# Kernel tuning notes

Hardware: AMD Instinct MI355X
Metric: run time of the kernel (lower is better)

The kernel has to match this reference:

```python
import jax, jax.numpy as jnp
import numpy as np
from jax import lax

SPARSE_TH = 0.01
STRIDE = (1, 1)


def setup_inputs() -> dict:
    key = jax.random.key(0)
    k1, k2, k3 = jax.random.split(key, 3)
    x = jax.random.normal(k1, (32, 56, 56, 256), dtype=jnp.float32)  # NHWC
    # weight: (out_channels, in_channels, kh, kw); scale so a fraction falls below sparse_th
    weight = jax.random.normal(k2, (256, 256, 3, 3), dtype=jnp.float32) * 0.05
    bias = jax.random.normal(k3, (256,), dtype=jnp.float32)
    return {"x": x, "weight": weight, "bias": bias}


def reference(x, weight, bias):
    # Threshold weights: |w| < sparse_th -> 0 (the sparse kernel computes the
    # identical math as a dense valid conv with the masked weight)
    w = jnp.where(jnp.abs(weight) < SPARSE_TH, jnp.zeros_like(weight), weight)
    # OIHW -> HWIO for NHWC conv
    w_hwio = jnp.transpose(w, (2, 3, 1, 0))
    out = lax.conv_general_dilated(
        x, w_hwio,
        window_strides=STRIDE,
        padding="VALID",
        dimension_numbers=("NHWC", "HWIO", "NHWC"),
    )
    return out + bias.reshape(1, 1, 1, -1)
```

## Files before the change

### kernel.cpp

```cpp
#include <hip/hip_runtime.h>
#include <hip/hip_bf16.h>


typedef __bf16 bf16x8 __attribute__((ext_vector_type(8)));
typedef float f32x4 __attribute__((ext_vector_type(4)));

#define GLOBAL_AS __attribute__((address_space(1)))
#define LDS_AS __attribute__((address_space(3)))

static __device__ __forceinline__ void glds16(const void* g, void* l) {
    __builtin_amdgcn_global_load_lds((const GLOBAL_AS unsigned int*)g,
                                     (LDS_AS unsigned int*)l, 16, 0, 0);
}

static __device__ __forceinline__ unsigned short f2bf(float f) {
    unsigned int u = __float_as_uint(f);
    unsigned int r = u + 0x7FFFu + ((u >> 16) & 1u);
    return (unsigned short)(r >> 16);
}

__global__ void cvt_xw(const float* __restrict__ x, unsigned short* __restrict__ xb,
                       const float* __restrict__ w, unsigned short* __restrict__ wt) {
    const int NXB = 32 * 56 * 56 * 256 / (256 * 8);
    if (blockIdx.x < NXB) {
        int i = (blockIdx.x * 256 + threadIdx.x) * 8;
        const float4* p = (const float4*)(x + i);
        float4 a = p[0], b = p[1];
        uint4 v;
        v.x = (unsigned)f2bf(a.x) | ((unsigned)f2bf(a.y) << 16);
        v.y = (unsigned)f2bf(a.z) | ((unsigned)f2bf(a.w) << 16);
        v.z = (unsigned)f2bf(b.x) | ((unsigned)f2bf(b.y) << 16);
        v.w = (unsigned)f2bf(b.z) | ((unsigned)f2bf(b.w) << 16);
        *(uint4*)(xb + i) = v;
    } else {
        int co = blockIdx.x - NXB;
        int ci = threadIdx.x;
        const float* src = w + co * 2304 + ci * 9;
        unsigned short* dst = wt + co * 2304 + ci;
#pragma unroll
        for (int khw = 0; khw < 9; ++khw) {
            float v = src[khw];
            v = (fabsf(v) < 0.01f) ? 0.0f : v;
            dst[khw * 256] = f2bf(v);
        }
    }
}

static __device__ __forceinline__ int swz_key(int row16) {
    return (row16 & 3) ^ ((row16 >> 2) & 3);
}

__global__ __launch_bounds__(512, 2) void conv_gemm(
    const unsigned short* __restrict__ Xb,
    const unsigned short* __restrict__ Wt,
    const float* __restrict__ bias,
    float* __restrict__ Out)
{
    __shared__ __align__(16) unsigned short As[4][128 * 32];
    __shared__ __align__(16) unsigned short Bs[4][256 * 32];

    const int tid  = threadIdx.x;
    const int lane = tid & 63;
    const int wave = tid >> 6;

    const int m0 = blockIdx.x * 128;

    const int arow = tid >> 2;
    const int ach  = (tid & 3) ^ swz_key(arow & 15);
    int am = m0 + arow;
    int an = am / 2916;
    int arem = am - an * 2916;
    int aoh = arem / 54;
    int aow = arem - aoh * 54;
    const unsigned short* a_base =
        Xb + (((an * 56 + aoh) * 56 + aow) << 8) + ach * 8;

    const int s1 = 512 + tid;
    const int br0 = tid >> 2, br1 = s1 >> 2;
    const unsigned short* b_base0 =
        Wt + br0 * 2304 + (((tid & 3) ^ swz_key(br0 & 15)) << 3);
    const unsigned short* b_base1 =
        Wt + br1 * 2304 + (((s1 & 3) ^ swz_key(br1 & 15)) << 3);

    const int fm = lane & 15;
    const int fq = lane >> 4;
    const int wm = (wave >> 2) * 64;
    const int wn = (wave & 3) * 64;
    const int slot8 = (fq ^ swz_key(fm)) * 8;

    f32x4 acc[4][4];
#pragma unroll
    for (int i = 0; i < 4; ++i)
#pragma unroll
        for (int j = 0; j < 4; ++j)
            acc[i][j] = (f32x4){0.f, 0.f, 0.f, 0.f};

#pragma unroll
    for (int tp = 0; tp < 3; ++tp) {
        glds16(a_base + tp * 32, &As[tp][wave * 512]);
        glds16(b_base0 + tp * 32, &Bs[tp][wave * 512]);
        glds16(b_base1 + tp * 32, &Bs[tp][4096 + wave * 512]);
    }
    asm volatile("s_waitcnt vmcnt(6)\n\ts_barrier" ::: "memory");

#pragma unroll 1
    for (int t = 0; t < 72; ++t) {
        const int b = t & 3;
        const unsigned short* Ab = As[b];
        const unsigned short* Bb = Bs[b];
        bf16x8 af[4], bfr[4];
#pragma unroll
        for (int mi = 0; mi < 4; ++mi)
            af[mi] = *(const bf16x8*)&Ab[(wm + mi * 16 + fm) * 32 + slot8];
#pragma unroll
        for (int ni = 0; ni < 4; ++ni)
            bfr[ni] = *(const bf16x8*)&Bb[(wn + ni * 16 + fm) * 32 + slot8];

        const int tn = t + 3;
        if (tn < 72) {
            const int bn = tn & 3;
            const int khw = tn >> 3;
            const int kh = (khw * 11) >> 5;
            const int kw = khw - kh * 3;
            const int aoff = ((kh * 56 + kw) << 8) + (tn & 7) * 32;
            const int boff = tn * 32;
            glds16(a_base + aoff, &As[bn][wave * 512]);
            glds16(b_base0 + boff, &Bs[bn][wave * 512]);
            glds16(b_base1 + boff, &Bs[bn][4096 + wave * 512]);
        }

        __builtin_amdgcn_s_setprio(1);
#pragma unroll
        for (int mi = 0; mi < 4; ++mi)
#pragma unroll
            for (int ni = 0; ni < 4; ++ni)
                acc[mi][ni] = __builtin_amdgcn_mfma_f32_16x16x32_bf16(
                    af[mi], bfr[ni], acc[mi][ni], 0, 0, 0);
        __builtin_amdgcn_s_setprio(0);

        if (t < 69) asm volatile("s_waitcnt vmcnt(6)\n\ts_barrier" ::: "memory");
        else        asm volatile("s_waitcnt vmcnt(0)\n\ts_barrier" ::: "memory");
    }

    float bv[4];
#pragma unroll
    for (int ni = 0; ni < 4; ++ni) bv[ni] = bias[wn + ni * 16 + fm];
#pragma unroll
    for (int mi = 0; mi < 4; ++mi) {
#pragma unroll
        for (int reg = 0; reg < 4; ++reg) {
            int m = m0 + wm + mi * 16 + fq * 4 + reg;
            float* orow = Out + m * 256 + wn + fm;
#pragma unroll
            for (int ni = 0; ni < 4; ++ni)
                orow[ni * 16] = acc[mi][ni][reg] + bv[ni];
        }
    }
}

extern "C" void kernel_launch(void* const* d_in, const int* in_sizes, int n_in,
                              void* d_out, int out_size, void* d_ws, size_t ws_size,
                              hipStream_t stream) {
    const float* x    = (const float*)d_in[0];
    const float* w    = (const float*)d_in[1];
    const float* bias = (const float*)d_in[2];
    float* out = (float*)d_out;

    const int NX = 32 * 56 * 56 * 256;
    unsigned short* xb = (unsigned short*)d_ws;
    unsigned short* wt = xb + NX;

    cvt_xw<<<NX / (256 * 8) + 256, 256, 0, stream>>>(x, xb, w, wt);
    conv_gemm<<<729, 512, 0, stream>>>(xb, wt, bias, out);
}
```

Before: 299.5 us.

## Store tiles in MFMA fragment order in LDS and use grid-stride conversion

The GEMM kernel now has each thread load a global chunk so that LDS holds the data already in the MFMA fragment layout. Each lane then reads its fragment at a contiguous lane*8 offset, which replaces the XOR swizzle addressing and should avoid bank conflicts. The prefetch for stage t+3 is moved ahead of the LDS fragment reads. The conversion kernel switches to a grid-stride loop over 2048 blocks using float4 to ushort4 stores, in place of one block per 2048 elements. A risk is that global loads become less coalesced, since each group of 4 lanes now touches a different row.

```diff
diff --git a/kernel.cpp b/kernel.cpp
--- a/kernel.cpp
+++ b/kernel.cpp
@@ -19,21 +19,22 @@
     return (unsigned short)(r >> 16);
 }
 
-__global__ void cvt_xw(const float* __restrict__ x, unsigned short* __restrict__ xb,
-                       const float* __restrict__ w, unsigned short* __restrict__ wt) {
-    const int NXB = 32 * 56 * 56 * 256 / (256 * 8);
-    if (blockIdx.x < NXB) {
-        int i = (blockIdx.x * 256 + threadIdx.x) * 8;
-        const float4* p = (const float4*)(x + i);
-        float4 a = p[0], b = p[1];
-        uint4 v;
-        v.x = (unsigned)f2bf(a.x) | ((unsigned)f2bf(a.y) << 16);
-        v.y = (unsigned)f2bf(a.z) | ((unsigned)f2bf(a.w) << 16);
-        v.z = (unsigned)f2bf(b.x) | ((unsigned)f2bf(b.y) << 16);
-        v.w = (unsigned)f2bf(b.z) | ((unsigned)f2bf(b.w) << 16);
-        *(uint4*)(xb + i) = v;
+__global__ __launch_bounds__(256) void cvt_xw(
+    const float* __restrict__ x, unsigned short* __restrict__ xb,
+    const float* __restrict__ w, unsigned short* __restrict__ wt) {
+    if (blockIdx.x < 2048) {
+        const int NV4 = 32 * 56 * 56 * 256 / 4;
+        const int stride = 2048 * 256;
+        const float4* __restrict__ src = (const float4*)x;
+        ushort4* __restrict__ dst = (ushort4*)xb;
+        for (int j = blockIdx.x * 256 + threadIdx.x; j < NV4; j += stride) {
+            float4 a = src[j];
+            ushort4 o;
+            o.x = f2bf(a.x); o.y = f2bf(a.y); o.z = f2bf(a.z); o.w = f2bf(a.w);
+            dst[j] = o;
+        }
     } else {
-        int co = blockIdx.x - NXB;
+        int co = blockIdx.x - 2048;
         int ci = threadIdx.x;
         const float* src = w + co * 2304 + ci * 9;
         unsigned short* dst = wt + co * 2304 + ci;
@@ -44,10 +45,6 @@
             dst[khw * 256] = f2bf(v);
         }
     }
-}
-
-static __device__ __forceinline__ int swz_key(int row16) {
-    return (row16 & 3) ^ ((row16 >> 2) & 3);
 }
 
 __global__ __launch_bounds__(512, 2) void conv_gemm(
@@ -65,28 +62,26 @@
 
     const int m0 = blockIdx.x * 128;
 
-    const int arow = tid >> 2;
-    const int ach  = (tid & 3) ^ swz_key(arow & 15);
-    int am = m0 + arow;
+    const int sfm = tid & 15;
+    const int sfq = (tid >> 4) & 3;
+    int am = m0 + wave * 16 + sfm;
     int an = am / 2916;
     int arem = am - an * 2916;
     int aoh = arem / 54;
     int aow = arem - aoh * 54;
     const unsigned short* a_base =
-        Xb + (((an * 56 + aoh) * 56 + aow) << 8) + ach * 8;
+        Xb + (((an * 56 + aoh) * 56 + aow) << 8) + sfq * 8;
 
-    const int s1 = 512 + tid;
-    const int br0 = tid >> 2, br1 = s1 >> 2;
-    const unsigned short* b_base0 =
-        Wt + br0 * 2304 + (((tid & 3) ^ swz_key(br0 & 15)) << 3);
-    const unsigned short* b_base1 =
-        Wt + br1 * 2304 + (((s1 & 3) ^ swz_key(br1 & 15)) << 3);
+    const int bco0 = wave * 16 + sfm;
+    const unsigned short* b_base0 = Wt + bco0 * 2304 + sfq * 8;
+    const unsigned short* b_base1 = Wt + (bco0 + 128) * 2304 + sfq * 8;
 
     const int fm = lane & 15;
     const int fq = lane >> 4;
     const int wm = (wave >> 2) * 64;
     const int wn = (wave & 3) * 64;
-    const int slot8 = (fq ^ swz_key(fm)) * 8;
+    const int abase = (wave >> 2) * 2048;
+    const int bbase = (wave & 3) * 2048;
 
     f32x4 acc[4][4];
 #pragma unroll
@@ -95,12 +90,20 @@
         for (int j = 0; j < 4; ++j)
             acc[i][j] = (f32x4){0.f, 0.f, 0.f, 0.f};
 
+    auto stage = [&](int tn) {
+        const int bn = tn & 3;
+        const int khw = tn >> 3;
+        const int kh = (khw * 11) >> 5;
+        const int kw = khw - kh * 3;
+        const int aoff = ((kh * 56 + kw) << 8) + (tn & 7) * 32;
+        const int boff = tn * 32;
+        glds16(a_base + aoff, &As[bn][wave * 512]);
+        glds16(b_base0 + boff, &Bs[bn][wave * 512]);
+        glds16(b_base1 + boff, &Bs[bn][4096 + wave * 512]);
+    };
+
 #pragma unroll
-    for (int tp = 0; tp < 3; ++tp) {
-        glds16(a_base + tp * 32, &As[tp][wave * 512]);
-        glds16(b_base0 + tp * 32, &Bs[tp][wave * 512]);
-        glds16(b_base1 + tp * 32, &Bs[tp][4096 + wave * 512]);
-    }
+    for (int tp = 0; tp < 3; ++tp) stage(tp);
     asm volatile("s_waitcnt vmcnt(6)\n\ts_barrier" ::: "memory");
 
 #pragma unroll 1
@@ -108,26 +111,16 @@
         const int b = t & 3;
         const unsigned short* Ab = As[b];
         const unsigned short* Bb = Bs[b];
+
+        if (t + 3 < 72) stage(t + 3);
+
         bf16x8 af[4], bfr[4];
 #pragma unroll
         for (int mi = 0; mi < 4; ++mi)
-            af[mi] = *(const bf16x8*)&Ab[(wm + mi * 16 + fm) * 32 + slot8];
+            af[mi] = *(const bf16x8*)&Ab[abase + mi * 512 + lane * 8];
 #pragma unroll
         for (int ni = 0; ni < 4; ++ni)
-            bfr[ni] = *(const bf16x8*)&Bb[(wn + ni * 16 + fm) * 32 + slot8];
-
-        const int tn = t + 3;
-        if (tn < 72) {
-            const int bn = tn & 3;
-            const int khw = tn >> 3;
-            const int kh = (khw * 11) >> 5;
-            const int kw = khw - kh * 3;
-            const int aoff = ((kh * 56 + kw) << 8) + (tn & 7) * 32;
-            const int boff = tn * 32;
-            glds16(a_base + aoff, &As[bn][wave * 512]);
-            glds16(b_base0 + boff, &Bs[bn][wave * 512]);
-            glds16(b_base1 + boff, &Bs[bn][4096 + wave * 512]);
-        }
+            bfr[ni] = *(const bf16x8*)&Bb[bbase + ni * 512 + lane * 8];
 
         __builtin_amdgcn_s_setprio(1);
 #pragma unroll
@@ -170,6 +163,6 @@
     unsigned short* xb = (unsigned short*)d_ws;
     unsigned short* wt = xb + NX;
 
-    cvt_xw<<<NX / (256 * 8) + 256, 256, 0, stream>>>(x, xb, w, wt);
+    cvt_xw<<<2304, 256, 0, stream>>>(x, xb, w, wt);
     conv_gemm<<<729, 512, 0, stream>>>(xb, wt, bias, out);
 }
```

Result: slower. 418.7 us (+39.8%).
